# Kernel optimization log

Hardware: AMD Instinct MI355X
Metric: run time of the kernel (lower is better)

The kernel has to match this reference:

```python
import jax, jax.numpy as jnp
import numpy as np

L, N, D = 4, 50000, 64        # lookback, n_nodes, gnn_dim
E = 500000                    # n_edges
HID = 256
LN_EPS = 1e-5


def setup_inputs() -> dict:
    key = jax.random.key(0)
    ks = jax.random.split(key, 8)
    h_all = jax.random.normal(ks[0], (L, N, D), dtype=jnp.float32)
    src = jax.random.randint(ks[1], (E,), 0, N, dtype=jnp.int32)
    dst = jax.random.randint(ks[2], (E,), 0, N, dtype=jnp.int32)
    W1 = jax.random.normal(ks[3], (HID, L * 2 * D), dtype=jnp.float32) * (1.0 / np.sqrt(L * 2 * D))
    b1 = jax.random.normal(ks[4], (HID,), dtype=jnp.float32) * 0.01
    W3 = jax.random.normal(ks[5], (1, HID), dtype=jnp.float32) * (1.0 / np.sqrt(HID))
    b3 = jax.random.normal(ks[6], (1,), dtype=jnp.float32) * 0.01
    gamma2 = jnp.ones((HID,), dtype=jnp.float32)
    beta2 = jnp.zeros((HID,), dtype=jnp.float32)
    return {"h_all": h_all, "src": src, "dst": dst, "W1": W1, "b1": b1,
            "W3": W3, "b3": b3, "gamma2": gamma2, "beta2": beta2}


def reference(h_all, src, dst, W1, b1, W3, b3, gamma2, beta2):
    lb, _, d = h_all.shape
    # importance weights 1..L normalized
    imp = jnp.arange(1, lb + 1, dtype=h_all.dtype)
    imp = imp / imp.sum()
    # per-edge gather of src/dst features for every lookback step: [L, E, 2D]
    hs = h_all[:, src]                                  # [L, E, D]
    hd = h_all[:, dst]                                  # [L, E, D]
    embed = jnp.concatenate([hs, hd], axis=-1) * imp[:, None, None]
    # concat over lookback steps -> [E, L*2D]
    embed = jnp.transpose(embed, (1, 0, 2)).reshape(embed.shape[1], -1)
    # MLP: W1(tanh) -> LayerNorm -> dropout(eval=identity) -> relu -> W3
    x = jnp.tanh(embed) @ W1.T + b1                     # [E, HID]
    mu = jnp.mean(x, axis=-1, keepdims=True)
    var = jnp.var(x, axis=-1, keepdims=True)
    x = (x - mu) * jax.lax.rsqrt(var + LN_EPS) * gamma2 + beta2
    x = jax.nn.relu(x)
    out = x @ W3.T + b3                                 # [E, 1]
    return out[:, 0]
```

## Files before the change

kernel.cpp:

```cpp
#include <hip/hip_runtime.h>
#include <hip/hip_bf16.h>

#define LL 4
#define NN 50000
#define DD 64
#define EE 500000
#define HID 256
#define KDIM 512
#define LN_EPS 1e-5f

typedef __bf16 bf16x8 __attribute__((ext_vector_type(8)));
typedef float f32x16 __attribute__((ext_vector_type(16)));

__device__ __forceinline__ void async16(const void* g, void* l) {
    __builtin_amdgcn_global_load_lds(
        (const __attribute__((address_space(1))) void*)g,
        (__attribute__((address_space(3))) void*)l, 16, 0, 0);
}

__global__ void tanh_conv(const float* __restrict__ h, __bf16* __restrict__ t) {
    int i = (blockIdx.x * 256 + threadIdx.x) * 8;
    int l = i / (NN * DD);
    float imp = (float)(l + 1) * 0.1f;
    const float4* p = (const float4*)(h + i);
    float4 a = p[0];
    float4 b = p[1];
    float x[8] = {a.x, a.y, a.z, a.w, b.x, b.y, b.z, b.w};
    bf16x8 r;
    #pragma unroll
    for (int j = 0; j < 8; ++j) {
        float e2 = __expf(2.0f * (imp * x[j]));
        r[j] = (__bf16)(1.0f - 2.0f / (e2 + 1.0f));
    }
    *(bf16x8*)(t + i) = r;
}

__global__ void w2_conv(const float* __restrict__ w1, __bf16* __restrict__ o) {
    int t = blockIdx.x * 256 + threadIdx.x;
    int j  = t & 511;
    int b  = t >> 9;
    int k0 = (b >> 1) * 16 + (b & 1) * 8;
    int r  = j & 255;
    int col = (k0 >> 6) * 128 + ((j >> 8) ? 64 : 0) + (k0 & 63);
    const float4* p = (const float4*)(w1 + r * KDIM + col);
    float4 va = p[0];
    float4 vb = p[1];
    bf16x8 v;
    v[0] = (__bf16)va.x; v[1] = (__bf16)va.y; v[2] = (__bf16)va.z; v[3] = (__bf16)va.w;
    v[4] = (__bf16)vb.x; v[5] = (__bf16)vb.y; v[6] = (__bf16)vb.z; v[7] = (__bf16)vb.w;
    *(bf16x8*)(o + (size_t)t * 8) = v;
}

__global__ __launch_bounds__(256, 2)
void node_proj(const __bf16* __restrict__ tb, const __bf16* __restrict__ w2c,
               __bf16* __restrict__ P) {
    __shared__ __align__(16) char smem[65536];
    __bf16* Bs = (__bf16*)smem;
    float*  Cs = (float*)smem;

    const int tid  = threadIdx.x;
    const int wave = tid >> 6;
    const int lane = tid & 63;
    const int h32  = lane >> 5;
    const int c32  = lane & 31;
    const int cb   = blockIdx.y;
    const int n00  = blockIdx.x * 128;

    #pragma unroll
    for (int it = 0; it < 16; ++it) {
        int o = it * 2048 + tid * 8;
        async16(w2c + (size_t)(o >> 10) * 4096 + cb * 1024 + (o & 1023), Bs + o);
    }

    int node = n00 + wave * 32 + c32;
    if (node >= NN) node = NN - 1;
    uint4 a[16];
    #pragma unroll
    for (int u = 0; u < 16; ++u) {
        const __bf16* p = tb + (size_t)(u >> 2) * (NN * DD) + node * DD
                        + (u & 3) * 16 + h32 * 8;
        a[u] = *(const uint4*)p;
    }

    f32x16 acc[4];
    #pragma unroll
    for (int nt = 0; nt < 4; ++nt) acc[nt] = (f32x16)(0.f);

    __syncthreads();

    #pragma unroll
    for (int u = 0; u < 16; ++u) {
        bf16x8 af = __builtin_bit_cast(bf16x8, a[u]);
        const __bf16* Bk = Bs + (u * 2 + h32) * 1024 + c32 * 8;
        #pragma unroll
        for (int nt = 0; nt < 4; ++nt) {
            bf16x8 bf = *(const bf16x8*)(Bk + nt * 256);
            acc[nt] = __builtin_amdgcn_mfma_f32_32x32x16_bf16(af, bf, acc[nt], 0, 0, 0);
        }
    }
    __syncthreads();

    #pragma unroll
    for (int nt = 0; nt < 4; ++nt) {
        #pragma unroll
        for (int r = 0; r < 16; ++r) {
            int nl = wave * 32 + (r & 3) + 8 * (r >> 2) + 4 * h32;
            Cs[nl * 128 + nt * 32 + c32] = acc[nt][r];
        }
    }
    __syncthreads();
    #pragma unroll
    for (int it = 0; it < 8; ++it) {
        int o  = it * 2048 + tid * 8;
        int nl = o >> 7;
        int n  = n00 + nl;
        if (n < NN) {
            bf16x8 v;
            #pragma unroll
            for (int z = 0; z < 8; ++z) v[z] = (__bf16)Cs[o + z];
            *(bf16x8*)(P + (size_t)n * 512 + cb * 128 + (o & 127)) = v;
        }
    }
}

__global__ __launch_bounds__(256, 3)
void edge_out(const __bf16* __restrict__ P, const int* __restrict__ src,
              const int* __restrict__ dst, const float* __restrict__ b1,
              const float* __restrict__ w3, const float* __restrict__ b3,
              const float* __restrict__ gamma, const float* __restrict__ beta,
              float* __restrict__ out) {
    const int tid = threadIdx.x;
    const int g   = tid >> 4;
    const int j   = tid & 15;

    float b1v[16], gv[16], btv[16], wv[16];
    {
        const float4* pb = (const float4*)(b1 + j * 16);
        const float4* pg = (const float4*)(gamma + j * 16);
        const float4* pt = (const float4*)(beta + j * 16);
        const float4* pw = (const float4*)(w3 + j * 16);
        #pragma unroll
        for (int z = 0; z < 4; ++z) {
            float4 vb = pb[z], vg = pg[z], vt = pt[z], vw = pw[z];
            b1v[z*4+0] = vb.x; b1v[z*4+1] = vb.y; b1v[z*4+2] = vb.z; b1v[z*4+3] = vb.w;
            gv [z*4+0] = vg.x; gv [z*4+1] = vg.y; gv [z*4+2] = vg.z; gv [z*4+3] = vg.w;
            btv[z*4+0] = vt.x; btv[z*4+1] = vt.y; btv[z*4+2] = vt.z; btv[z*4+3] = vt.w;
            wv [z*4+0] = vw.x; wv [z*4+1] = vw.y; wv [z*4+2] = vw.z; wv [z*4+3] = vw.w;
        }
    }
    const float b3v = b3[0];
    const int e0 = blockIdx.x * 128 + g * 8;

    uint4 cs0, cs1, cd0, cd1, ns0, ns1, nd0, nd1;
    {
        int ec = e0 < EE ? e0 : EE - 1;
        int s = src[ec], d = dst[ec];
        const uint4* ps = (const uint4*)(P + (size_t)s * 512 + j * 16);
        const uint4* pd = (const uint4*)(P + (size_t)d * 512 + 256 + j * 16);
        cs0 = ps[0]; cs1 = ps[1]; cd0 = pd[0]; cd1 = pd[1];
    }
    #pragma unroll
    for (int i = 0; i < 8; ++i) {
        if (i < 7) {
            int e = e0 + i + 1;
            int ec = e < EE ? e : EE - 1;
            int s = src[ec], d = dst[ec];
            const uint4* ps = (const uint4*)(P + (size_t)s * 512 + j * 16);
            const uint4* pd = (const uint4*)(P + (size_t)d * 512 + 256 + j * 16);
            ns0 = ps[0]; ns1 = ps[1]; nd0 = pd[0]; nd1 = pd[1];
        }
        bf16x8 a0 = __builtin_bit_cast(bf16x8, cs0);
        bf16x8 a1 = __builtin_bit_cast(bf16x8, cs1);
        bf16x8 c0 = __builtin_bit_cast(bf16x8, cd0);
        bf16x8 c1 = __builtin_bit_cast(bf16x8, cd1);
        float x[16];
        #pragma unroll
        for (int z = 0; z < 8; ++z) {
            x[z]     = (float)a0[z] + (float)c0[z] + b1v[z];
            x[z + 8] = (float)a1[z] + (float)c1[z] + b1v[z + 8];
        }
        float sum = 0.f, sq = 0.f;
        #pragma unroll
        for (int z = 0; z < 16; ++z) {
            sum += x[z];
            sq   = fmaf(x[z], x[z], sq);
        }
        #pragma unroll
        for (int m = 1; m < 16; m <<= 1) {
            sum += __shfl_xor(sum, m);
            sq  += __shfl_xor(sq,  m);
        }
        float mu = sum * (1.0f / 256.0f);
        float rs = rsqrtf(sq * (1.0f / 256.0f) - mu * mu + LN_EPS);
        float dot = 0.f;
        #pragma unroll
        for (int z = 0; z < 16; ++z) {
            float y = fmaxf((x[z] - mu) * rs * gv[z] + btv[z], 0.f);
            dot = fmaf(y, wv[z], dot);
        }
        #pragma unroll
        for (int m = 1; m < 16; m <<= 1) dot += __shfl_xor(dot, m);
        int e = e0 + i;
        if (j == 0 && e < EE) out[e] = dot + b3v;
        cs0 = ns0; cs1 = ns1; cd0 = nd0; cd1 = nd1;
    }
}

extern "C" void kernel_launch(void* const* d_in, const int* in_sizes, int n_in,
                              void* d_out, int out_size, void* d_ws, size_t ws_size,
                              hipStream_t stream) {
    const float* h_all  = (const float*)d_in[0];
    const int*   src    = (const int*)  d_in[1];
    const int*   dst    = (const int*)  d_in[2];
    const float* W1     = (const float*)d_in[3];
    const float* b1     = (const float*)d_in[4];
    const float* W3     = (const float*)d_in[5];
    const float* b3     = (const float*)d_in[6];
    const float* gamma2 = (const float*)d_in[7];
    const float* beta2  = (const float*)d_in[8];
    float* out = (float*)d_out;

    __bf16* tb  = (__bf16*)d_ws;
    __bf16* w2c = tb + (size_t)LL * NN * DD;
    __bf16* P   = w2c + 131072;

    tanh_conv<<<6250, 256, 0, stream>>>(h_all, tb);
    w2_conv<<<64, 256, 0, stream>>>(W1, w2c);
    node_proj<<<dim3((NN + 127) / 128, 4), 256, 0, stream>>>(tb, w2c, P);
    edge_out<<<(EE + 127) / 128, 256, 0, stream>>>(P, src, dst, b1, W3, b3,
                                                   gamma2, beta2, out);
}
```

Baseline: 202.6 us.

## Fold bias into node projections and cut edge kernel register pressure

The b1 bias is split in half and added to both the src and dst node projections in node_proj, so edge_out no longer keeps b1 in registers. edge_out now loads the src/dst indices once per group, spread across lanes, and broadcasts them with shuffles. It also drops the software double-buffered prefetch and raises launch bounds from 3 to 5 blocks per SM to hide gather latency through occupancy. The tradeoff is less explicit prefetching, plus extra bf16 rounding because the bias is added before the conversion to bf16.

```diff
diff --git a/kernel.cpp b/kernel.cpp
--- a/kernel.cpp
+++ b/kernel.cpp
@@ -53,7 +53,7 @@
 
 __global__ __launch_bounds__(256, 2)
 void node_proj(const __bf16* __restrict__ tb, const __bf16* __restrict__ w2c,
-               __bf16* __restrict__ P) {
+               const float* __restrict__ b1, __bf16* __restrict__ P) {
     __shared__ __align__(16) char smem[65536];
     __bf16* Bs = (__bf16*)smem;
     float*  Cs = (float*)smem;
@@ -115,34 +115,34 @@
         int nl = o >> 7;
         int n  = n00 + nl;
         if (n < NN) {
+            int hbase = ((cb & 1) << 7) | (o & 127);
             bf16x8 v;
             #pragma unroll
-            for (int z = 0; z < 8; ++z) v[z] = (__bf16)Cs[o + z];
+            for (int z = 0; z < 8; ++z)
+                v[z] = (__bf16)(Cs[o + z] + 0.5f * b1[hbase + z]);
             *(bf16x8*)(P + (size_t)n * 512 + cb * 128 + (o & 127)) = v;
         }
     }
 }
 
-__global__ __launch_bounds__(256, 3)
+__global__ __launch_bounds__(256, 5)
 void edge_out(const __bf16* __restrict__ P, const int* __restrict__ src,
-              const int* __restrict__ dst, const float* __restrict__ b1,
-              const float* __restrict__ w3, const float* __restrict__ b3,
-              const float* __restrict__ gamma, const float* __restrict__ beta,
-              float* __restrict__ out) {
+              const int* __restrict__ dst, const float* __restrict__ w3,
+              const float* __restrict__ b3, const float* __restrict__ gamma,
+              const float* __restrict__ beta, float* __restrict__ out) {
     const int tid = threadIdx.x;
     const int g   = tid >> 4;
     const int j   = tid & 15;
-
-    float b1v[16], gv[16], btv[16], wv[16];
+    const int lb  = (g & 3) << 4;
+
+    float gv[16], btv[16], wv[16];
     {
-        const float4* pb = (const float4*)(b1 + j * 16);
         const float4* pg = (const float4*)(gamma + j * 16);
         const float4* pt = (const float4*)(beta + j * 16);
         const float4* pw = (const float4*)(w3 + j * 16);
         #pragma unroll
         for (int z = 0; z < 4; ++z) {
-            float4 vb = pb[z], vg = pg[z], vt = pt[z], vw = pw[z];
-            b1v[z*4+0] = vb.x; b1v[z*4+1] = vb.y; b1v[z*4+2] = vb.z; b1v[z*4+3] = vb.w;
+            float4 vg = pg[z], vt = pt[z], vw = pw[z];
             gv [z*4+0] = vg.x; gv [z*4+1] = vg.y; gv [z*4+2] = vg.z; gv [z*4+3] = vg.w;
             btv[z*4+0] = vt.x; btv[z*4+1] = vt.y; btv[z*4+2] = vt.z; btv[z*4+3] = vt.w;
             wv [z*4+0] = vw.x; wv [z*4+1] = vw.y; wv [z*4+2] = vw.z; wv [z*4+3] = vw.w;
@@ -151,33 +151,28 @@
     const float b3v = b3[0];
     const int e0 = blockIdx.x * 128 + g * 8;
 
-    uint4 cs0, cs1, cd0, cd1, ns0, ns1, nd0, nd1;
-    {
-        int ec = e0 < EE ? e0 : EE - 1;
-        int s = src[ec], d = dst[ec];
-        const uint4* ps = (const uint4*)(P + (size_t)s * 512 + j * 16);
-        const uint4* pd = (const uint4*)(P + (size_t)d * 512 + 256 + j * 16);
-        cs0 = ps[0]; cs1 = ps[1]; cd0 = pd[0]; cd1 = pd[1];
-    }
+    int ej = e0 + (j & 7);
+    if (ej >= EE) ej = EE - 1;
+    const int sv = src[ej];
+    const int dv = dst[ej];
+
     #pragma unroll
     for (int i = 0; i < 8; ++i) {
-        if (i < 7) {
-            int e = e0 + i + 1;
-            int ec = e < EE ? e : EE - 1;
-            int s = src[ec], d = dst[ec];
-            const uint4* ps = (const uint4*)(P + (size_t)s * 512 + j * 16);
-            const uint4* pd = (const uint4*)(P + (size_t)d * 512 + 256 + j * 16);
-            ns0 = ps[0]; ns1 = ps[1]; nd0 = pd[0]; nd1 = pd[1];
-        }
-        bf16x8 a0 = __builtin_bit_cast(bf16x8, cs0);
-        bf16x8 a1 = __builtin_bit_cast(bf16x8, cs1);
-        bf16x8 c0 = __builtin_bit_cast(bf16x8, cd0);
-        bf16x8 c1 = __builtin_bit_cast(bf16x8, cd1);
+        const int s = __shfl(sv, lb + i);
+        const int d = __shfl(dv, lb + i);
+        const uint4* ps = (const uint4*)(P + ((size_t)s << 9) + (j << 4));
+        const uint4* pd = (const uint4*)(P + ((size_t)d << 9) + 256 + (j << 4));
+        uint4 rs0 = ps[0], rs1 = ps[1];
+        uint4 rd0 = pd[0], rd1 = pd[1];
+        bf16x8 A0 = __builtin_bit_cast(bf16x8, rs0);
+        bf16x8 A1 = __builtin_bit_cast(bf16x8, rs1);
+        bf16x8 C0 = __builtin_bit_cast(bf16x8, rd0);
+        bf16x8 C1 = __builtin_bit_cast(bf16x8, rd1);
         float x[16];
         #pragma unroll
         for (int z = 0; z < 8; ++z) {
-            x[z]     = (float)a0[z] + (float)c0[z] + b1v[z];
-            x[z + 8] = (float)a1[z] + (float)c1[z] + b1v[z + 8];
+            x[z]     = (float)A0[z] + (float)C0[z];
+            x[z + 8] = (float)A1[z] + (float)C1[z];
         }
         float sum = 0.f, sq = 0.f;
         #pragma unroll
@@ -195,14 +190,14 @@
         float dot = 0.f;
         #pragma unroll
         for (int z = 0; z < 16; ++z) {
-            float y = fmaxf((x[z] - mu) * rs * gv[z] + btv[z], 0.f);
+            float t = (x[z] - mu) * rs;
+            float y = fmaxf(fmaf(t, gv[z], btv[z]), 0.f);
             dot = fmaf(y, wv[z], dot);
         }
         #pragma unroll
         for (int m = 1; m < 16; m <<= 1) dot += __shfl_xor(dot, m);
         int e = e0 + i;
         if (j == 0 && e < EE) out[e] = dot + b3v;
-        cs0 = ns0; cs1 = ns1; cd0 = nd0; cd1 = nd1;
     }
 }
 
@@ -226,7 +221,7 @@
 
     tanh_conv<<<6250, 256, 0, stream>>>(h_all, tb);
     w2_conv<<<64, 256, 0, stream>>>(W1, w2c);
-    node_proj<<<dim3((NN + 127) / 128, 4), 256, 0, stream>>>(tb, w2c, P);
-    edge_out<<<(EE + 127) / 128, 256, 0, stream>>>(P, src, dst, b1, W3, b3,
+    node_proj<<<dim3((NN + 127) / 128, 4), 256, 0, stream>>>(tb, w2c, b1, P);
+    edge_out<<<(EE + 127) / 128, 256, 0, stream>>>(P, src, dst, W3, b3,
                                                    gamma2, beta2, out);
 }
```

Result: slower. 211.3 us (+4.3%).
